# Kernel optimization log

Hardware: AMD Instinct MI355X
Metric: run time of the kernel (lower is better)

The kernel has to match this reference:

```python
import jax, jax.numpy as jnp
import numpy as np

K = 3  # kernel size from init_kwargs


def setup_inputs() -> dict:
    key = jax.random.key(0)
    x = jax.random.normal(key, (16, K * K, 512, 512), dtype=jnp.float32)
    return {"x": x}


def reference(x) -> jnp.ndarray:
    # Faithful col2im / fold: conv_transpose2d with identity-channel weight,
    # stride=1, padding=K//2. Channel c = i*K + j contributes tap (i,j):
    #   out[b, p, q] = sum_{i,j} x[b, i*K+j, p - (i - pad), q - (j - pad)]
    # Implemented as 9 static shifted-slice adds (no wasted zero multiplies).
    k = K
    pad = k // 2
    b, c, h, w = x.shape
    xp = jnp.pad(x, ((0, 0), (0, 0), (pad, pad), (pad, pad)))  # [b, k^2, h+2p, w+2p]
    out = jnp.zeros((b, h, w), dtype=x.dtype)
    for i in range(k):
        for j in range(k):
            ch = i * k + j
            ri = 2 * pad - i  # row slice start
            cj = 2 * pad - j  # col slice start
            out = out + xp[:, ch, ri:ri + h, cj:cj + w]
    return out[:, None, :, :]  # [b, 1, h, w]
```

## Files before the change

kernel.cpp:

```cpp
#include <hip/hip_runtime.h>


constexpr int B = 16;
constexpr int C = 9;
constexpr int H = 512;
constexpr int W = 512;
constexpr int WV = W / 4;

typedef float f4_u __attribute__((ext_vector_type(4), aligned(4)));

__global__ __launch_bounds__(256) void fold_kernel(const float* __restrict__ x,
                                                   float* __restrict__ out) {
    const int tid = blockIdx.x * blockDim.x + threadIdx.x;
    const int qv = tid % WV;
    const int t2 = tid / WV;
    const int p  = t2 % H;
    const int b  = t2 / H;
    const int q0 = qv * 4;

    const size_t plane = (size_t)H * W;
    const float* xb = x + (size_t)b * C * plane;

    float ax = 0.f, ay = 0.f, az = 0.f, aw = 0.f;
    const bool interior = (qv != 0) & (qv != WV - 1);

#pragma unroll
    for (int i = 0; i < 3; ++i) {
        const int r = p + 1 - i;
        if (r < 0 || r >= H) continue;
#pragma unroll
        for (int j = 0; j < 3; ++j) {
            const float* xrow = xb + (size_t)(i * 3 + j) * plane + (size_t)r * W;
            const int c0 = q0 + 1 - j;
            if (interior) {
                f4_u v = *reinterpret_cast<const f4_u*>(xrow + c0);
                ax += v.x; ay += v.y; az += v.z; aw += v.w;
            } else {
                if (c0 >= 0 && c0 < W)         ax += xrow[c0];
                if (c0 + 1 >= 0 && c0 + 1 < W) ay += xrow[c0 + 1];
                if (c0 + 2 >= 0 && c0 + 2 < W) az += xrow[c0 + 2];
                if (c0 + 3 >= 0 && c0 + 3 < W) aw += xrow[c0 + 3];
            }
        }
    }

    f4_u r;
    r.x = ax; r.y = ay; r.z = az; r.w = aw;
    *reinterpret_cast<f4_u*>(out + (size_t)tid * 4) = r;
}

extern "C" void kernel_launch(void* const* d_in, const int* in_sizes, int n_in,
                              void* d_out, int out_size, void* d_ws, size_t ws_size,
                              hipStream_t stream) {
    const float* x = (const float*)d_in[0];
    float* out = (float*)d_out;
    const int n_threads = B * H * WV;
    const int block = 256;
    const int grid = n_threads / block;
    fold_kernel<<<grid, block, 0, stream>>>(x, out);
}
```

Baseline: 209.0 us.

## Map one wavefront per output row with aligned loads and lane shuffles

Each 64-lane wavefront now computes one full output row, with every lane producing 8 consecutive outputs. All loads become 16-byte-aligned vector loads at the lane's own offset. The one-column shifts across neighbouring lanes are done with __shfl_down/__shfl_up instead of misaligned or per-element boundary loads. This removes the unaligned-access and divergent edge paths and doubles per-thread work, at the cost of cross-lane shuffle operations and fewer threads overall.

```diff
diff --git a/kernel.cpp b/kernel.cpp
--- a/kernel.cpp
+++ b/kernel.cpp
@@ -5,48 +5,56 @@
 constexpr int C = 9;
 constexpr int H = 512;
 constexpr int W = 512;
-constexpr int WV = W / 4;
 
-typedef float f4_u __attribute__((ext_vector_type(4), aligned(4)));
+typedef float f4 __attribute__((ext_vector_type(4)));
 
 __global__ __launch_bounds__(256) void fold_kernel(const float* __restrict__ x,
                                                    float* __restrict__ out) {
-    const int tid = blockIdx.x * blockDim.x + threadIdx.x;
-    const int qv = tid % WV;
-    const int t2 = tid / WV;
-    const int p  = t2 % H;
-    const int b  = t2 / H;
-    const int q0 = qv * 4;
+    const int gtid = blockIdx.x * blockDim.x + threadIdx.x;
+    const int row  = gtid >> 6;
+    const int lane = threadIdx.x & 63;
+    const int p = row & (H - 1);
+    const int b = row >> 9;
+    const int q0 = lane * 8;
 
     const size_t plane = (size_t)H * W;
     const float* xb = x + (size_t)b * C * plane;
 
-    float ax = 0.f, ay = 0.f, az = 0.f, aw = 0.f;
-    const bool interior = (qv != 0) & (qv != WV - 1);
+    float acc0 = 0.f, acc1 = 0.f, acc2 = 0.f, acc3 = 0.f;
+    float acc4 = 0.f, acc5 = 0.f, acc6 = 0.f, acc7 = 0.f;
 
 #pragma unroll
     for (int i = 0; i < 3; ++i) {
         const int r = p + 1 - i;
         if (r < 0 || r >= H) continue;
-#pragma unroll
-        for (int j = 0; j < 3; ++j) {
-            const float* xrow = xb + (size_t)(i * 3 + j) * plane + (size_t)r * W;
-            const int c0 = q0 + 1 - j;
-            if (interior) {
-                f4_u v = *reinterpret_cast<const f4_u*>(xrow + c0);
-                ax += v.x; ay += v.y; az += v.z; aw += v.w;
-            } else {
-                if (c0 >= 0 && c0 < W)         ax += xrow[c0];
-                if (c0 + 1 >= 0 && c0 + 1 < W) ay += xrow[c0 + 1];
-                if (c0 + 2 >= 0 && c0 + 2 < W) az += xrow[c0 + 2];
-                if (c0 + 3 >= 0 && c0 + 3 < W) aw += xrow[c0 + 3];
-            }
-        }
+        const float* base = xb + (size_t)(3 * i) * plane + (size_t)r * W + q0;
+
+        const f4 a0 = *reinterpret_cast<const f4*>(base);
+        const f4 a1 = *reinterpret_cast<const f4*>(base + 4);
+        const f4 b0 = *reinterpret_cast<const f4*>(base + plane);
+        const f4 b1 = *reinterpret_cast<const f4*>(base + plane + 4);
+        const f4 c0 = *reinterpret_cast<const f4*>(base + 2 * plane);
+        const f4 c1 = *reinterpret_cast<const f4*>(base + 2 * plane + 4);
+
+        acc0 += b0.x; acc1 += b0.y; acc2 += b0.z; acc3 += b0.w;
+        acc4 += b1.x; acc5 += b1.y; acc6 += b1.z; acc7 += b1.w;
+
+        acc0 += a0.y; acc1 += a0.z; acc2 += a0.w; acc3 += a1.x;
+        acc4 += a1.y; acc5 += a1.z; acc6 += a1.w;
+        const float nx = __shfl_down(a0.x, 1);
+        acc7 += (lane == 63) ? 0.f : nx;
+
+        const float pw = __shfl_up(c1.w, 1);
+        acc0 += (lane == 0) ? 0.f : pw;
+        acc1 += c0.x; acc2 += c0.y; acc3 += c0.z; acc4 += c0.w;
+        acc5 += c1.x; acc6 += c1.y; acc7 += c1.z;
     }
 
-    f4_u r;
-    r.x = ax; r.y = ay; r.z = az; r.w = aw;
-    *reinterpret_cast<f4_u*>(out + (size_t)tid * 4) = r;
+    float* orow = out + (size_t)row * W + q0;
+    f4 o0; o0.x = acc0; o0.y = acc1; o0.z = acc2; o0.w = acc3;
+    f4 o1; o1.x = acc4; o1.y = acc5; o1.z = acc6; o1.w = acc7;
+    *reinterpret_cast<f4*>(orow)     = o0;
+    *reinterpret_cast<f4*>(orow + 4) = o1;
 }
 
 extern "C" void kernel_launch(void* const* d_in, const int* in_sizes, int n_in,
@@ -54,8 +62,8 @@
                               hipStream_t stream) {
     const float* x = (const float*)d_in[0];
     float* out = (float*)d_out;
-    const int n_threads = B * H * WV;
-    const int block = 256;
-    const int grid = n_threads / block;
+    const int n_waves  = B * H;
+    const int block    = 256;
+    const int grid     = n_waves * 64 / block;
     fold_kernel<<<grid, block, 0, stream>>>(x, out);
 }
```

New measurement: 211.2 us. Within noise of the previous version (+1.0%).
